# Kernel tuning notes

Measured on AMD Instinct MI355X. Metric: run time of the kernel, lower is better.

The kernel has to match this reference:

```python
import jax, jax.numpy as jnp
import numpy as np

D_MODEL = 384
N_HEADS = 8
HEAD_DIM = D_MODEL // N_HEADS


def setup_inputs() -> dict:
    key = jax.random.key(0)
    ks = jax.random.split(key, 8)
    b, n = 2, 2048
    s = 0.02
    return {
        "x": jax.random.normal(ks[0], (b, n, D_MODEL), jnp.float32),
        "coords": jax.random.normal(ks[1], (b, n, 3), jnp.float32),
        "W_qkv": jax.random.normal(ks[2], (D_MODEL, 3 * D_MODEL), jnp.float32) * s,
        "b_qkv": jnp.zeros((3 * D_MODEL,), jnp.float32),
        "W_dist": jax.random.normal(ks[3], (1, N_HEADS), jnp.float32) * s,
        "b_dist": jnp.zeros((N_HEADS,), jnp.float32),
        "W_out": jax.random.normal(ks[4], (D_MODEL, D_MODEL), jnp.float32) * s,
        "b_out": jnp.zeros((D_MODEL,), jnp.float32),
    }


def reference(x, coords, W_qkv, b_qkv, W_dist, b_dist, W_out, b_out):
    b, n, _ = x.shape
    qkv = x @ W_qkv + b_qkv                       # (b, n, 3*d)
    q, k, v = jnp.split(qkv, 3, axis=-1)
    def heads(t):
        return t.reshape(b, n, N_HEADS, HEAD_DIM).transpose(0, 2, 1, 3)  # b h n d
    q, k, v = heads(q), heads(k), heads(v)
    attn = jnp.einsum('bhid,bhjd->bhij', q, k) / jnp.sqrt(jnp.float32(HEAD_DIM))
    # distance bias: ||c_i - c_j|| projected to heads (Linear(1, n_heads))
    diff = coords[:, :, None, :] - coords[:, None, :, :]   # (b, i, j, 3)
    dist = jnp.sqrt(jnp.sum(diff * diff, axis=-1))         # (b, i, j)
    dist_bias = dist[..., None] * W_dist[0] + b_dist       # (b, i, j, h)
    attn = attn + dist_bias.transpose(0, 3, 1, 2)          # (b, h, i, j)
    attn = jax.nn.softmax(attn, axis=-1)
    out = jnp.einsum('bhij,bhjd->bhid', attn, v)
    out = out.transpose(0, 2, 1, 3).reshape(b, n, D_MODEL)
    return out @ W_out + b_out
```

## Files before the change

### kernel.cpp

```cpp
#include <hip/hip_runtime.h>
#include <hip/hip_bf16.h>

#define NB 2
#define SEQ 2048
#define DM 384
#define NH 8
#define HD 48
#define QKVN 1152
#define BH (NB*NH)
#define NSPLIT 4

typedef __hip_bfloat16 bf16;
typedef __attribute__((ext_vector_type(8))) short short8;
typedef __attribute__((ext_vector_type(4))) float float4v;

static __device__ __forceinline__ float bf2f(bf16 v){ return __bfloat162float(v); }
static __device__ __forceinline__ float ldin(const void* p, size_t i, int isf){
    return isf ? ((const float*)p)[i] : bf2f(((const bf16*)p)[i]);
}
static __device__ __forceinline__ short f2b(float f){
    union { float f; unsigned u; } a; a.f = f;
    unsigned r = a.u + 0x7FFFu + ((a.u >> 16) & 1u);
    return (short)(r >> 16);
}
static __device__ __forceinline__ unsigned pk2(float a, float b){
    union { float f; unsigned u; } ua, ub; ua.f = a; ub.f = b;
    return ((ua.u + 0x8000u) >> 16) | ((ub.u + 0x8000u) & 0xFFFF0000u);
}
static __device__ __forceinline__ float bflo(unsigned u){
    union { unsigned u; float f; } a; a.u = u << 16; return a.f;
}
static __device__ __forceinline__ float bfhi(unsigned u){
    union { unsigned u; float f; } a; a.u = u & 0xFFFF0000u; return a.f;
}
static __device__ __forceinline__ short8 s4z(int2 v){
    union { int2 i; short s[4]; } u; u.i = v;
    short8 r = {u.s[0], u.s[1], u.s[2], u.s[3], 0, 0, 0, 0};
    return r;
}
static __device__ __forceinline__ short8 u2z(unsigned a, unsigned b){
    union { unsigned u[2]; short s[4]; } u0; u0.u[0] = a; u0.u[1] = b;
    short8 r = {u0.s[0], u0.s[1], u0.s[2], u0.s[3], 0, 0, 0, 0};
    return r;
}
static __device__ __forceinline__ int detect_isf(const void* x){
    const unsigned short* xb = (const unsigned short*)x;
    int l = threadIdx.x & 63;
    union { unsigned u; float f; } a; a.u = ((unsigned)xb[2*l]) << 16;
    float ab = fabsf(a.f);
    int good = (a.f == 0.0f) || (ab > 9.765625e-4f && ab < 1024.0f);
    unsigned long long m = __ballot(good);
    return (__popcll(m) >= 32) ? 0 : 1;
}

__global__ __launch_bounds__(256) void k_prep(const void* __restrict__ x,
    const void* __restrict__ coords,
    const void* __restrict__ Wqkv, const void* __restrict__ Wout,
    const void* __restrict__ bqkv, const void* __restrict__ bout,
    const void* __restrict__ Wdist, const void* __restrict__ bdist,
    short* __restrict__ dist8, short* __restrict__ xb,
    short* __restrict__ WqT, short* __restrict__ WoT,
    float* __restrict__ bqf, float* __restrict__ bof,
    float* __restrict__ wdf, float* __restrict__ bdf)
{
    const int isf = detect_isf(x);
    const int t = threadIdx.x;
    const int b = blockIdx.x;
    if (b < 512) {
        const int bb = b >> 8;
        const int jg = (b >> 1) & 127;
        const int j0 = jg * 16;
        const int ih = (b & 1) * 1024;
        __shared__ float cjx[16], cjy[16], cjz[16];
        if (t < 16) {
            int gj = (bb*SEQ + j0 + t)*3;
            cjx[t] = ldin(coords, gj, isf);
            cjy[t] = ldin(coords, gj+1, isf);
            cjz[t] = ldin(coords, gj+2, isf);
        }
        __syncthreads();
        #pragma unroll
        for (int k = 0; k < 4; ++k) {
            int i = ih + k*256 + t;
            int gi = (bb*SEQ + i)*3;
            float px = ldin(coords, gi, isf), py = ldin(coords, gi+1, isf), pz = ldin(coords, gi+2, isf);
            short o[16];
            #pragma unroll
            for (int e = 0; e < 16; ++e) {
                float dx = px - cjx[e], dy = py - cjy[e], dz = pz - cjz[e];
                o[e] = f2b(sqrtf(dx*dx + dy*dy + dz*dz));
            }
            short* dst = dist8 + (((size_t)bb*128 + jg)*SEQ + i)*16;
            *(int4*)dst       = *(const int4*)(o);
            *(int4*)(dst + 8) = *(const int4*)(o + 8);
        }
    } else if (b < 1280) {
        size_t i = ((size_t)(b-512)*256 + t)*8;
        if (isf) {
            const float* xf = (const float*)x + i;
            short o[8];
            #pragma unroll
            for (int e = 0; e < 8; ++e) o[e] = f2b(xf[e]);
            *(int4*)(xb + i) = *(const int4*)o;
        } else {
            *(int4*)(xb + i) = *(const int4*)((const short*)x + i);
        }
    } else if (b < 1856) {
        int bb, NW; const void* W; short* WT;
        if (b < 1712) { bb = b - 1280; NW = QKVN; W = Wqkv; WT = WqT; }
        else          { bb = b - 1712; NW = DM;   W = Wout; WT = WoT; }
        int ntiles = NW >> 5;
        int kt = bb / ntiles, nt = bb % ntiles;
        int k0 = kt*32, n0 = nt*32;
        __shared__ float Ls[32][33];
        for (int idx = t; idx < 1024; idx += 256) {
            int r = idx >> 5, c = idx & 31;
            Ls[r][c] = ldin(W, (size_t)(k0+r)*NW + n0 + c, isf);
        }
        __syncthreads();
        for (int idx = t; idx < 1024; idx += 256) {
            int r2 = idx >> 5, c2 = idx & 31;
            WT[(size_t)(n0+r2)*DM + k0 + c2] = f2b(Ls[c2][r2]);
        }
    } else {
        int idx = (b - 1856)*256 + t;
        const float log2e = 1.4426950408889634f;
        if (idx < QKVN) bqf[idx] = ldin(bqkv, idx, isf);
        else if (idx < QKVN + DM) bof[idx - QKVN] = ldin(bout, idx - QKVN, isf);
        else if (idx < QKVN + DM + NH) wdf[idx - QKVN - DM] = ldin(Wdist, idx - QKVN - DM, isf)*log2e;
        else if (idx < QKVN + DM + 2*NH) bdf[idx - QKVN - DM - NH] = ldin(bdist, idx - QKVN - DM - NH, isf)*log2e;
    }
}

__global__ __launch_bounds__(256) void k_qkv(const short* __restrict__ xb,
    const short* __restrict__ WT, const float* __restrict__ bias,
    short* __restrict__ qg2, short* __restrict__ kg2, short* __restrict__ vg2)
{
    __shared__ __align__(16) short As[64*72];
    __shared__ __align__(16) short Bs[128*72];
    const int t = threadIdx.x;
    const int w = t >> 6, lane = t & 63, L = lane & 15, quad = lane >> 4;
    const int mt = blockIdx.x / 9, nt = blockIdx.x % 9;
    const int row0 = mt*64, col0 = nt*128;
    const int wm = w & 1, wn = w >> 1;
    float4v acc[2][4] = {};
    for (int k0 = 0; k0 < DM; k0 += 64) {
        __syncthreads();
        for (int c = t; c < 512; c += 256) {
            int row = c >> 3, k8 = c & 7;
            *(int4*)(&As[row*72 + k8*8]) = *(const int4*)(xb + (size_t)(row0+row)*DM + k0 + k8*8);
        }
        for (int c = t; c < 1024; c += 256) {
            int row = c >> 3, k8 = c & 7;
            *(int4*)(&Bs[row*72 + k8*8]) = *(const int4*)(WT + (size_t)(col0+row)*DM + k0 + k8*8);
        }
        __syncthreads();
        #pragma unroll
        for (int kc = 0; kc < 2; ++kc) {
            short8 a0 = *(const short8*)(&As[(32*wm + L)*72 + kc*32 + quad*8]);
            short8 a1 = *(const short8*)(&As[(32*wm + 16 + L)*72 + kc*32 + quad*8]);
            #pragma unroll
            for (int ni = 0; ni < 4; ++ni) {
                short8 bf = *(const short8*)(&Bs[(64*wn + 16*ni + L)*72 + kc*32 + quad*8]);
                acc[0][ni] = __builtin_amdgcn_mfma_f32_16x16x32_bf16(a0, bf, acc[0][ni], 0, 0, 0);
                acc[1][ni] = __builtin_amdgcn_mfma_f32_16x16x32_bf16(a1, bf, acc[1][ni], 0, 0, 0);
            }
        }
    }
    const int which = col0 / DM;
    const int cbase = col0 % DM;
    short* Ep = Bs;
    __syncthreads();
    if (which < 2) {
        #pragma unroll
        for (int mi = 0; mi < 2; ++mi)
            #pragma unroll
            for (int ni = 0; ni < 4; ++ni) {
                int col_l = 64*wn + 16*ni + L;
                float bv = bias[col0 + col_l];
                #pragma unroll
                for (int r = 0; r < 4; ++r) {
                    int row_l = 32*wm + 16*mi + quad*4 + r;
                    Ep[row_l*136 + col_l] = f2b(acc[mi][ni][r] + bv);
                }
            }
        __syncthreads();
        short* dst = which ? kg2 : qg2;
        for (int c = t; c < 1024; c += 256) {
            int row_l = c >> 4, col_l = (c & 15)*8;
            int row_g = row0 + row_l;
            int bi = row_g >> 11, nn = row_g & (SEQ-1);
            int c2 = cbase + col_l;
            int hh = c2/HD, dh = c2%HD;
            int bh = bi*NH + hh;
            size_t base = ((size_t)bh*128 + (nn>>4))*768;
            int Ltok = nn & 15;
            const short* src = &Ep[row_l*136 + col_l];
            if (dh < 32) {
                *(int4*)(dst + base + (dh>>3)*128 + Ltok*8) = *(const int4*)src;
            } else {
                int q0 = (dh - 32) >> 2;
                *(int2*)(dst + base + 512 + q0*64     + Ltok*4) = *(const int2*)src;
                *(int2*)(dst + base + 512 + (q0+1)*64 + Ltok*4) = *(const int2*)(src + 4);
            }
        }
    } else {
        #pragma unroll
        for (int mi = 0; mi < 2; ++mi)
            #pragma unroll
            for (int ni = 0; ni < 4; ++ni) {
                int col_l = 64*wn + 16*ni + L;
                float bv = bias[col0 + col_l];
                #pragma unroll
                for (int r = 0; r < 4; ++r) {
                    int row_l = 32*wm + 16*mi + quad*4 + r;
                    Ep[col_l*72 + row_l] = f2b(acc[mi][ni][r] + bv);
                }
            }
        __syncthreads();
        for (int c = t; c < 1024; c += 256) {
            int col_l = c >> 3, row8 = (c & 7)*8;
            int row_g = row0 + row8;
            int bi = row_g >> 11, nn = row_g & (SEQ-1);
            int c2 = cbase + col_l;
            int hh = c2/HD, dh = c2%HD;
            int bh = bi*NH + hh;
            int dt = dh >> 4, Lh = dh & 15;
            size_t base3 = (((size_t)bh*128 + (nn>>4))*3 + dt)*256;
            int q0 = (nn & 15) >> 2;
            const short* src = &Ep[col_l*72 + row8];
            *(int2*)(vg2 + base3 + q0*64     + Lh*4) = *(const int2*)src;
            *(int2*)(vg2 + base3 + (q0+1)*64 + Lh*4) = *(const int2*)(src + 4);
        }
    }
}

__global__ __launch_bounds__(256, 4) void k_attn(
    const short* __restrict__ qg2, const short* __restrict__ kg2, const short* __restrict__ vg2,
    const short* __restrict__ dist8, const float* __restrict__ wdf,
    const float* __restrict__ bdf, short* __restrict__ partO, float* __restrict__ partL)
{
    __shared__ float Ored[2][32*48];
    __shared__ float Lred[2][32];
    const int t = threadIdx.x;
    const int w = t >> 6, lane = t & 63, L = lane & 15, q = lane >> 4;
    const int bid = blockIdx.x;
    const int jsb = bid & 3, it = (bid >> 2) & 63, bh = bid >> 8;
    const int bi = bh >> 3, hh = bh & 7;
    const int i0 = it*32;
    const float scale2 = 0.14433756729740643f * 1.4426950408889634f;
    const float wd = wdf[hh], bd = bdf[hh];

    const short* qB = qg2 + ((size_t)bh*128 + it*2)*768;
    short8 qa0[2], qa1[2];
    #pragma unroll
    for (int nt = 0; nt < 2; ++nt) {
        qa0[nt] = *(const short8*)(qB + nt*768 + q*128 + L*8);
        qa1[nt] = s4z(*(const int2*)(qB + nt*768 + 512 + q*64 + L*4));
    }

    float4v accO[2][3] = {};
    float rsum[2] = {};

    const short* kBp = kg2 + ((size_t)bh*128 + jsb*32 + w)*768;
    const short* vBp = vg2 + ((size_t)bh*128 + jsb*32 + w)*768;
    const short* dBp = dist8 + (((size_t)bi*128 + jsb*32 + w)*SEQ + i0 + L)*16 + 4*q;

    #pragma unroll 2
    for (int itr = 0; itr < SEQ/NSPLIT/64; ++itr) {
        short8 ka0 = *(const short8*)(kBp + q*128 + L*8);
        short8 ka1 = s4z(*(const int2*)(kBp + 512 + q*64 + L*4));
        float4v sacc[2] = {};
        #pragma unroll
        for (int nt = 0; nt < 2; ++nt) {
            sacc[nt] = __builtin_amdgcn_mfma_f32_16x16x32_bf16(ka0, qa0[nt], sacc[nt], 0, 0, 0);
            sacc[nt] = __builtin_amdgcn_mfma_f32_16x16x32_bf16(ka1, qa1[nt], sacc[nt], 0, 0, 0);
        }
        short8 vf[3];
        #pragma unroll
        for (int dt = 0; dt < 3; ++dt)
            vf[dt] = s4z(*(const int2*)(vBp + dt*256 + q*64 + L*4));
        short8 pa[2];
        #pragma unroll
        for (int nt = 0; nt < 2; ++nt) {
            int2 du = *(const int2*)(dBp + nt*256);
            float d0 = bflo((unsigned)du.x), d1 = bfhi((unsigned)du.x);
            float d2 = bflo((unsigned)du.y), d3 = bfhi((unsigned)du.y);
            float p0 = __builtin_amdgcn_exp2f(fmaf(sacc[nt][0], scale2, fmaf(d0, wd, bd)));
            float p1 = __builtin_amdgcn_exp2f(fmaf(sacc[nt][1], scale2, fmaf(d1, wd, bd)));
            float p2 = __builtin_amdgcn_exp2f(fmaf(sacc[nt][2], scale2, fmaf(d2, wd, bd)));
            float p3 = __builtin_amdgcn_exp2f(fmaf(sacc[nt][3], scale2, fmaf(d3, wd, bd)));
            rsum[nt] += (p0 + p1) + (p2 + p3);
            pa[nt] = u2z(pk2(p0, p1), pk2(p2, p3));
        }
        #pragma unroll
        for (int nt = 0; nt < 2; ++nt)
            #pragma unroll
            for (int dt = 0; dt < 3; ++dt)
                accO[nt][dt] = __builtin_amdgcn_mfma_f32_16x16x32_bf16(pa[nt], vf[dt], accO[nt][dt], 0, 0, 0);
        kBp += 4*768; vBp += 4*768; dBp += (size_t)4*SEQ*16;
    }
    #pragma unroll
    for (int nt = 0; nt < 2; ++nt) {
        rsum[nt] += __shfl_xor(rsum[nt], 16);
        rsum[nt] += __shfl_xor(rsum[nt], 32);
    }
    if (w >= 2) {
        float* Od = Ored[w-2];
        #pragma unroll
        for (int mt = 0; mt < 2; ++mt)
            #pragma unroll
            for (int dt = 0; dt < 3; ++dt)
                #pragma unroll
                for (int r = 0; r < 4; ++r)
                    Od[(16*mt + 4*q + r)*48 + 16*dt + L] = accO[mt][dt][r];
        if (q == 0)
            #pragma unroll
            for (int nt = 0; nt < 2; ++nt) Lred[w-2][16*nt + L] = rsum[nt];
    }
    __syncthreads();
    if (w < 2) {
        float* Od = Ored[w];
        #pragma unroll
        for (int mt = 0; mt < 2; ++mt)
            #pragma unroll
            for (int dt = 0; dt < 3; ++dt)
                #pragma unroll
                for (int r = 0; r < 4; ++r)
                    accO[mt][dt][r] += Od[(16*mt + 4*q + r)*48 + 16*dt + L];
        #pragma unroll
        for (int nt = 0; nt < 2; ++nt) rsum[nt] += Lred[w][16*nt + L];
    }
    __syncthreads();
    if (w == 1) {
        float* Od = Ored[0];
        #pragma unroll
        for (int mt = 0; mt < 2; ++mt)
            #pragma unroll
            for (int dt = 0; dt < 3; ++dt)
                #pragma unroll
                for (int r = 0; r < 4; ++r)
                    Od[(16*mt + 4*q + r)*48 + 16*dt + L] = accO[mt][dt][r];
        if (q == 0)
            #pragma unroll
            for (int nt = 0; nt < 2; ++nt) Lred[0][16*nt + L] = rsum[nt];
    }
    __syncthreads();
    if (w == 0) {
        float* Od = Ored[0];
        const size_t pbase = ((size_t)(jsb*BH + bh))*SEQ;
        #pragma unroll
        for (int mt = 0; mt < 2; ++mt)
            #pragma unroll
            for (int dt = 0; dt < 3; ++dt)
                #pragma unroll
                for (int r = 0; r < 4; ++r) {
                    float v = accO[mt][dt][r] + Od[(16*mt + 4*q + r)*48 + 16*dt + L];
                    partO[(pbase + i0 + 16*mt + 4*q + r)*48 + 16*dt + L] = f2b(v);
                }
        if (q == 0)
            #pragma unroll
            for (int nt = 0; nt < 2; ++nt)
                partL[pbase + i0 + 16*nt + L] = rsum[nt] + Lred[0][16*nt + L];
    }
}

__global__ __launch_bounds__(256) void k_red(const short* __restrict__ partO,
    const float* __restrict__ partL, short* __restrict__ aob)
{
    int g = blockIdx.x*256 + threadIdx.x;
    int row = g / 48, cg = g % 48;
    int bi = row >> 11, i = row & (SEQ-1);
    int hh = cg / 6, d8 = (cg % 6)*8;
    int bh = bi*NH + hh;
    float acc[8] = {};
    float l = 0.f;
    #pragma unroll
    for (int s = 0; s < NSPLIT; ++s) {
        const short* p = partO + ((size_t)(s*BH + bh)*SEQ + i)*48 + d8;
        uint4 u = *(const uint4*)p;
        acc[0] += bflo(u.x); acc[1] += bfhi(u.x);
        acc[2] += bflo(u.y); acc[3] += bfhi(u.y);
        acc[4] += bflo(u.z); acc[5] += bfhi(u.z);
        acc[6] += bflo(u.w); acc[7] += bfhi(u.w);
        l += partL[(size_t)(s*BH + bh)*SEQ + i];
    }
    float inv = 1.0f / l;
    short o[8];
    #pragma unroll
    for (int e = 0; e < 8; ++e) o[e] = f2b(acc[e]*inv);
    *(int4*)(aob + (size_t)row*DM + hh*HD + d8) = *(const int4*)o;
}

__global__ __launch_bounds__(256) void k_out(const short* __restrict__ aob,
    const short* __restrict__ WT, const float* __restrict__ bias,
    void* __restrict__ out, const void* __restrict__ x)
{
    __shared__ __align__(16) short As[64*72];
    __shared__ __align__(16) short Bs[128*72];
    const int isf = detect_isf(x);
    const int t = threadIdx.x;
    const int w = t >> 6, lane = t & 63, L = lane & 15, quad = lane >> 4;
    const int mt = blockIdx.x / 3, nt = blockIdx.x % 3;
    const int row0 = mt*64, col0 = nt*128;
    const int wm = w & 1, wn = w >> 1;
    float4v acc[2][4] = {};
    for (int k0 = 0; k0 < DM; k0 += 64) {
        __syncthreads();
        for (int c = t; c < 512; c += 256) {
            int row = c >> 3, k8 = c & 7;
            *(int4*)(&As[row*72 + k8*8]) = *(const int4*)(aob + (size_t)(row0+row)*DM + k0 + k8*8);
        }
        for (int c = t; c < 1024; c += 256) {
            int row = c >> 3, k8 = c & 7;
            *(int4*)(&Bs[row*72 + k8*8]) = *(const int4*)(WT + (size_t)(col0+row)*DM + k0 + k8*8);
        }
        __syncthreads();
        #pragma unroll
        for (int kc = 0; kc < 2; ++kc) {
            short8 a0 = *(const short8*)(&As[(32*wm + L)*72 + kc*32 + quad*8]);
            short8 a1 = *(const short8*)(&As[(32*wm + 16 + L)*72 + kc*32 + quad*8]);
            #pragma unroll
            for (int ni = 0; ni < 4; ++ni) {
                short8 bf = *(const short8*)(&Bs[(64*wn + 16*ni + L)*72 + kc*32 + quad*8]);
                acc[0][ni] = __builtin_amdgcn_mfma_f32_16x16x32_bf16(a0, bf, acc[0][ni], 0, 0, 0);
                acc[1][ni] = __builtin_amdgcn_mfma_f32_16x16x32_bf16(a1, bf, acc[1][ni], 0, 0, 0);
            }
        }
    }
    #pragma unroll
    for (int mi = 0; mi < 2; ++mi) {
        #pragma unroll
        for (int ni = 0; ni < 4; ++ni) {
            int col_g = col0 + 64*wn + 16*ni + L;
            float bv = bias[col_g];
            #pragma unroll
            for (int r = 0; r < 4; ++r) {
                int row_g = row0 + 32*wm + 16*mi + quad*4 + r;
                size_t oi = (size_t)row_g*DM + col_g;
                float val = acc[mi][ni][r] + bv;
                if (isf) ((float*)out)[oi] = val;
                else     ((bf16*)out)[oi]  = __float2bfloat16(val);
            }
        }
    }
}

extern "C" void kernel_launch(void* const* d_in, const int* in_sizes, int n_in,
                              void* d_out, int out_size, void* d_ws, size_t ws_size,
                              hipStream_t stream) {
    const void* x      = d_in[0];
    const void* coords = d_in[1];
    const void* Wqkv   = d_in[2];
    const void* bqkv   = d_in[3];
    const void* Wdist  = d_in[4];
    const void* bdist  = d_in[5];
    const void* Wout   = d_in[6];
    const void* bout   = d_in[7];

    short* qg2   = (short*)d_ws;
    short* kg2   = qg2  + (size_t)1572864;
    short* vg2   = kg2  + (size_t)1572864;
    short* dist8 = vg2  + (size_t)1572864;
    short* aob   = dist8 + (size_t)8388608;
    short* xb    = aob  + (size_t)1572864;
    short* WqT   = xb   + (size_t)1572864;
    short* WoT   = WqT  + (size_t)442368;
    short* partO = WoT  + (size_t)147456;
    float* partL = (float*)(partO + (size_t)6291456);
    float* bqf   = partL + (size_t)131072;
    float* bof   = bqf + QKVN;
    float* wdf   = bof + DM;
    float* bdf   = wdf + NH;

    k_prep<<<dim3(1863), dim3(256), 0, stream>>>(x, coords, Wqkv, Wout, bqkv, bout,
                                                 Wdist, bdist, dist8, xb, WqT, WoT,
                                                 bqf, bof, wdf, bdf);
    k_qkv<<<dim3(64*9), dim3(256), 0, stream>>>(xb, WqT, bqf, qg2, kg2, vg2);
    k_attn<<<dim3(16*64*NSPLIT), dim3(256), 0, stream>>>(qg2, kg2, vg2, dist8, wdf, bdf,
                                                         partO, partL);
    k_red<<<dim3(768), dim3(256), 0, stream>>>(partO, partL, aob);
    k_out<<<dim3(64*3), dim3(256), 0, stream>>>(aob, WoT, bof, d_out, x);
}
```

Baseline: 160.2 us.

## Remove split-KV in attention and fuse normalization into attention kernel

Drops the 4-way split over the key dimension, so each attention block walks the full sequence and normalizes its own output in shared memory before writing the bf16 attention result directly. This removes the partial-output buffers, their global write and read traffic, and the separate reduction kernel launch. In exchange the attention grid shrinks from 4096 to 1024 blocks with four times longer serial loops per block, which lowers available parallelism and latency hiding on a GPU with many compute units.

New measurement: 153.6 us. -4.1%, faster.

```diff
diff --git a/kernel.cpp b/kernel.cpp
--- a/kernel.cpp
+++ b/kernel.cpp
@@ -8,7 +8,6 @@
 #define HD 48
 #define QKVN 1152
 #define BH (NB*NH)
-#define NSPLIT 4
 
 typedef __hip_bfloat16 bf16;
 typedef __attribute__((ext_vector_type(8))) short short8;
@@ -238,14 +237,14 @@
 __global__ __launch_bounds__(256, 4) void k_attn(
     const short* __restrict__ qg2, const short* __restrict__ kg2, const short* __restrict__ vg2,
     const short* __restrict__ dist8, const float* __restrict__ wdf,
-    const float* __restrict__ bdf, short* __restrict__ partO, float* __restrict__ partL)
+    const float* __restrict__ bdf, short* __restrict__ aob)
 {
     __shared__ float Ored[2][32*48];
     __shared__ float Lred[2][32];
     const int t = threadIdx.x;
     const int w = t >> 6, lane = t & 63, L = lane & 15, q = lane >> 4;
     const int bid = blockIdx.x;
-    const int jsb = bid & 3, it = (bid >> 2) & 63, bh = bid >> 8;
+    const int it = bid & 63, bh = bid >> 6;
     const int bi = bh >> 3, hh = bh & 7;
     const int i0 = it*32;
     const float scale2 = 0.14433756729740643f * 1.4426950408889634f;
@@ -262,12 +261,12 @@
     float4v accO[2][3] = {};
     float rsum[2] = {};
 
-    const short* kBp = kg2 + ((size_t)bh*128 + jsb*32 + w)*768;
-    const short* vBp = vg2 + ((size_t)bh*128 + jsb*32 + w)*768;
-    const short* dBp = dist8 + (((size_t)bi*128 + jsb*32 + w)*SEQ + i0 + L)*16 + 4*q;
+    const short* kBp = kg2 + ((size_t)bh*128 + w)*768;
+    const short* vBp = vg2 + ((size_t)bh*128 + w)*768;
+    const short* dBp = dist8 + (((size_t)bi*128 + w)*SEQ + i0 + L)*16 + 4*q;
 
     #pragma unroll 2
-    for (int itr = 0; itr < SEQ/NSPLIT/64; ++itr) {
+    for (int itr = 0; itr < SEQ/64; ++itr) {
         short8 ka0 = *(const short8*)(kBp + q*128 + L*8);
         short8 ka1 = s4z(*(const int2*)(kBp + 512 + q*64 + L*4));
         float4v sacc[2] = {};
@@ -348,48 +347,27 @@
     __syncthreads();
     if (w == 0) {
         float* Od = Ored[0];
-        const size_t pbase = ((size_t)(jsb*BH + bh))*SEQ;
         #pragma unroll
         for (int mt = 0; mt < 2; ++mt)
             #pragma unroll
             for (int dt = 0; dt < 3; ++dt)
                 #pragma unroll
-                for (int r = 0; r < 4; ++r) {
-                    float v = accO[mt][dt][r] + Od[(16*mt + 4*q + r)*48 + 16*dt + L];
-                    partO[(pbase + i0 + 16*mt + 4*q + r)*48 + 16*dt + L] = f2b(v);
-                }
+                for (int r = 0; r < 4; ++r)
+                    Od[(16*mt + 4*q + r)*48 + 16*dt + L] += accO[mt][dt][r];
         if (q == 0)
             #pragma unroll
-            for (int nt = 0; nt < 2; ++nt)
-                partL[pbase + i0 + 16*nt + L] = rsum[nt] + Lred[0][16*nt + L];
-    }
-}
-
-__global__ __launch_bounds__(256) void k_red(const short* __restrict__ partO,
-    const float* __restrict__ partL, short* __restrict__ aob)
-{
-    int g = blockIdx.x*256 + threadIdx.x;
-    int row = g / 48, cg = g % 48;
-    int bi = row >> 11, i = row & (SEQ-1);
-    int hh = cg / 6, d8 = (cg % 6)*8;
-    int bh = bi*NH + hh;
-    float acc[8] = {};
-    float l = 0.f;
-    #pragma unroll
-    for (int s = 0; s < NSPLIT; ++s) {
-        const short* p = partO + ((size_t)(s*BH + bh)*SEQ + i)*48 + d8;
-        uint4 u = *(const uint4*)p;
-        acc[0] += bflo(u.x); acc[1] += bfhi(u.x);
-        acc[2] += bflo(u.y); acc[3] += bfhi(u.y);
-        acc[4] += bflo(u.z); acc[5] += bfhi(u.z);
-        acc[6] += bflo(u.w); acc[7] += bfhi(u.w);
-        l += partL[(size_t)(s*BH + bh)*SEQ + i];
-    }
-    float inv = 1.0f / l;
-    short o[8];
-    #pragma unroll
-    for (int e = 0; e < 8; ++e) o[e] = f2b(acc[e]*inv);
-    *(int4*)(aob + (size_t)row*DM + hh*HD + d8) = *(const int4*)o;
+            for (int nt = 0; nt < 2; ++nt) Lred[0][16*nt + L] += rsum[nt];
+    }
+    __syncthreads();
+    for (int c = t; c < 192; c += 256) {
+        int r = c / 6, d8 = (c % 6)*8;
+        float inv = 1.0f / Lred[0][r];
+        const float* src = &Ored[0][r*48 + d8];
+        short o[8];
+        #pragma unroll
+        for (int e = 0; e < 8; ++e) o[e] = f2b(src[e]*inv);
+        *(int4*)(aob + ((size_t)(bi*SEQ) + i0 + r)*DM + hh*HD + d8) = *(const int4*)o;
+    }
 }
 
 __global__ __launch_bounds__(256) void k_out(const short* __restrict__ aob,
@@ -466,9 +444,7 @@
     short* xb    = aob  + (size_t)1572864;
     short* WqT   = xb   + (size_t)1572864;
     short* WoT   = WqT  + (size_t)442368;
-    short* partO = WoT  + (size_t)147456;
-    float* partL = (float*)(partO + (size_t)6291456);
-    float* bqf   = partL + (size_t)131072;
+    float* bqf   = (float*)(WoT + (size_t)147456);
     float* bof   = bqf + QKVN;
     float* wdf   = bof + DM;
     float* bdf   = wdf + NH;
@@ -477,8 +453,6 @@
                                                  Wdist, bdist, dist8, xb, WqT, WoT,
                                                  bqf, bof, wdf, bdf);
     k_qkv<<<dim3(64*9), dim3(256), 0, stream>>>(xb, WqT, bqf, qg2, kg2, vg2);
-    k_attn<<<dim3(16*64*NSPLIT), dim3(256), 0, stream>>>(qg2, kg2, vg2, dist8, wdf, bdf,
-                                                         partO, partL);
-    k_red<<<dim3(768), dim3(256), 0, stream>>>(partO, partL, aob);
+    k_attn<<<dim3(16*64), dim3(256), 0, stream>>>(qg2, kg2, vg2, dist8, wdf, bdf, aob);
     k_out<<<dim3(64*3), dim3(256), 0, stream>>>(aob, WoT, bof, d_out, x);
 }
```
